# Kernel optimization log

Hardware: AMD Instinct MI355X
Metric: run time of the kernel (lower is better)

Reference implementation:

```python
import jax, jax.numpy as jnp
import numpy as np

N = 131072       # total nodes (B graphs x P nodes)
P = 4096         # nodes per graph
B = 32           # graphs in batch
E = 2097152      # edges (avg degree 16)
IN_DIM = 64
HID = 128
OUT = 16
EPS = 1e-5
SLOPE = 0.01


def _degrees(idx):
    # structural degree, clamped to min 1 (as DGL GraphConv does)
    d = jax.ops.segment_sum(jnp.ones((E,), jnp.float32), idx, num_segments=N)
    return jnp.maximum(d, 1.0)


def _graph_conv(x, W, src, dst, ew):
    # DGL GraphConv, norm='both', bias=False, with scalar edge weights:
    # h = D_out^{-1/2} x ; m_v = sum_{(u->v)} w_e h_u ; out = (D_in^{-1/2} m) W
    h = x * jax.lax.rsqrt(_degrees(src))[:, None]
    m = jax.ops.segment_sum(ew[:, None] * h[src], dst, num_segments=N)  # [N, F]
    return (m * jax.lax.rsqrt(_degrees(dst))[:, None]) @ W


def _graph_norm(x, gamma, beta, alpha):
    # GraphNorm (Cai et al. / PyG, batch=None): stats over all nodes per feature
    mu = jnp.mean(x, axis=0)
    c = x - alpha * mu
    var = jnp.mean(c * c, axis=0)
    return c * jax.lax.rsqrt(var + EPS) * gamma + beta


def _mean_nodes(h, gid):
    # per-graph mean readout; every graph has exactly P nodes
    return jax.ops.segment_sum(h, gid, num_segments=B) / P


def setup_inputs() -> dict:
    key = jax.random.key(0)
    ks = jax.random.split(key, 8)
    src = jax.random.randint(ks[0], (E,), 0, N, dtype=jnp.int32)
    # keep edges within each 4096-node graph block (batched DGL graph)
    dst = (src // P) * P + jax.random.randint(ks[1], (E,), 0, P, dtype=jnp.int32)
    features = jax.random.normal(ks[2], (N, IN_DIM), jnp.float32)
    edge_weights = jax.random.uniform(ks[3], (E,), jnp.float32)
    # kaiming/xavier-scale init approximations
    W1 = jax.random.normal(ks[4], (IN_DIM, HID), jnp.float32) * np.sqrt(2.0 / IN_DIM)
    W2 = jax.random.normal(ks[5], (HID, HID), jnp.float32) * np.sqrt(2.0 / HID)
    Wc = jax.random.normal(ks[6], (OUT, 2 * HID), jnp.float32) * np.sqrt(1.0 / (2 * HID))
    ones = jnp.ones((HID,), jnp.float32)
    zeros = jnp.zeros((HID,), jnp.float32)
    return {
        'features': features, 'edge_weights': edge_weights, 'src': src, 'dst': dst,
        'W1': W1, 'W2': W2, 'Wc': Wc,
        'gamma1': ones, 'beta1': zeros, 'alpha1': ones,
        'gamma2': ones, 'beta2': zeros, 'alpha2': ones,
    }


def reference(features, edge_weights, src, dst, W1, W2, Wc,
              gamma1, beta1, alpha1, gamma2, beta2, alpha2):
    gid = jnp.arange(N, dtype=jnp.int32) // P  # node -> graph id
    h1 = _graph_conv(features, W1, src, dst, edge_weights)
    h1 = jax.nn.leaky_relu(_graph_norm(h1, gamma1, beta1, alpha1), SLOPE)
    r1 = _mean_nodes(h1, gid)                  # [B, HID]
    h2 = _graph_conv(h1, W2, src, dst, edge_weights)
    h2 = jax.nn.leaky_relu(_graph_norm(h2, gamma2, beta2, alpha2), SLOPE)
    r2 = _mean_nodes(h2, gid)                  # [B, HID]
    readouts = jnp.concatenate([r1, r2], axis=1)  # [B, 2*HID]
    return readouts @ Wc.T                     # [B, OUT]
```

## Files before the change

### kernel.cpp

```cpp
#include <hip/hip_runtime.h>
#include <hip/hip_fp16.h>

constexpr int NN   = 131072;
constexpr int PP   = 4096;
constexpr int BG   = 32;
constexpr int EE   = 2097152;
constexpr int IND  = 64;
constexpr int HH   = 128;
constexpr int CAP  = 81920;
constexpr float EPSV   = 1e-5f;
constexpr float SLOPEV = 0.01f;

typedef short bf16x8 __attribute__((ext_vector_type(8)));
typedef float f32x4  __attribute__((ext_vector_type(4)));
typedef float f32x2  __attribute__((ext_vector_type(2)));

__device__ __forceinline__ unsigned f2bf(float f) {
    unsigned u = __float_as_uint(f);
    return (u + 0x7FFFu + ((u >> 16) & 1u)) >> 16;
}
__device__ __forceinline__ unsigned pack2bf(float lo, float hi) {
    return f2bf(lo) | (f2bf(hi) << 16);
}
__device__ __forceinline__ float bflo(unsigned p) { return __uint_as_float(p << 16); }
__device__ __forceinline__ float bfhi(unsigned p) { return __uint_as_float(p & 0xFFFF0000u); }
__device__ __forceinline__ float w16(unsigned r) {
    return __half2float(__ushort_as_half((unsigned short)(r >> 16)));
}

template <int K>
__device__ __forceinline__ void packw_body(const float* __restrict__ W,
                                           unsigned short* __restrict__ pw, int t) {
    if (t >= K * 16) return;
    int lane = t & 63, nt = (t >> 6) & 7, kt = t >> 9;
    int kbase = kt * 32 + ((lane >> 4) & 3) * 8;
    int col   = nt * 16 + (lane & 15);
    for (int j = 0; j < 8; j++)
        pw[t * 8 + j] = (unsigned short)f2bf(W[(kbase + j) * HH + col]);
}

__global__ __launch_bounds__(256) void k_prep(const float* __restrict__ features,
                                              unsigned* __restrict__ f8x,
                                              const float* __restrict__ W1,
                                              unsigned short* __restrict__ pw1,
                                              const float* __restrict__ W2,
                                              unsigned short* __restrict__ pw2,
                                              int* __restrict__ gcur,
                                              float* __restrict__ racc,
                                              unsigned* __restrict__ csr2) {
    int b = blockIdx.x, t = threadIdx.x;
    if (b < 8192) {
        int i = b * 256 + t;
        float4 v = ((const float4*)features)[i];
        int w0 = __builtin_amdgcn_cvt_pk_fp8_f32(v.x, v.y, 0, false);
        int w1 = __builtin_amdgcn_cvt_pk_fp8_f32(v.z, v.w, w0, true);
        f8x[i] = (unsigned)w1;
        return;
    }
    if (b == 8192) {
        if (t < BG) gcur[t * 16] = t * CAP;
        for (int i = t; i < 2 * BG * HH; i += 256) racc[i] = 0.f;
        return;
    }
    if (b < 8197) { packw_body<64>(W1, pw1, (b - 8193) * 256 + t); return; }
    if (b < 8205) { packw_body<128>(W2, pw2, (b - 8197) * 256 + t); return; }
    ((uint4*)csr2)[(b - 8205) * 256 + t] = make_uint4(0, 0, 0, 0);
}

__global__ __launch_bounds__(256) void k_part(const int* __restrict__ src,
                                              const int* __restrict__ dst,
                                              const float* __restrict__ ew,
                                              int* __restrict__ gcur,
                                              uint2* __restrict__ recs) {
    __shared__ int cnt[32];
    __shared__ int start[32];
    __shared__ int gbase[32];
    __shared__ uint2 stage[4096];
    int t = threadIdx.x;
    int ebase = blockIdx.x * 4096;
    if (t < 32) cnt[t] = 0;
    __syncthreads();
    int es[16]; int ed[16]; float ev[16];
#pragma unroll
    for (int k = 0; k < 16; k++) {
        int e = ebase + k * 256 + t;
        es[k] = src[e]; ed[k] = dst[e]; ev[k] = ew[e];
        atomicAdd(&cnt[es[k] >> 12], 1);
    }
    __syncthreads();
    if (t == 0) {
        int run = 0;
        for (int g = 0; g < 32; g++) { start[g] = run; run += cnt[g]; }
    }
    __syncthreads();
    if (t < 32) {
        gbase[t] = atomicAdd(&gcur[t * 16], cnt[t]);
        cnt[t] = start[t];
    }
    __syncthreads();
#pragma unroll
    for (int k = 0; k < 16; k++) {
        int g = es[k] >> 12;
        int pos = atomicAdd(&cnt[g], 1);
        stage[pos] = make_uint2((unsigned)(es[k] & 4095) | ((unsigned)(ed[k] & 4095) << 12) |
                                ((unsigned)g << 24), __float_as_uint(ev[k]));
    }
    __syncthreads();
    for (int i = t; i < 4096; i += 256) {
        uint2 r = stage[i];
        int g = r.x >> 24;
        recs[gbase[g] + (i - start[g])] = r;
    }
}

__global__ __launch_bounds__(1024) void k_hist(const uint2* __restrict__ recs,
                                               const int* __restrict__ gcur,
                                               int* __restrict__ shist,
                                               int* __restrict__ dhist) {
    __shared__ int hs[4096];
    __shared__ int hd[4096];
    int t = threadIdx.x;
    int g = blockIdx.x >> 3, c = blockIdx.x & 7;
    int n = gcur[g * 16] - g * CAP;
    int lo = (n * c) >> 3, hi = (n * (c + 1)) >> 3;
    ((int4*)hs)[t] = make_int4(0, 0, 0, 0);
    ((int4*)hd)[t] = make_int4(0, 0, 0, 0);
    __syncthreads();
    const uint2* base = recs + (size_t)g * CAP;
    for (int i = lo + t; i < hi; i += 1024) {
        unsigned x = base[i].x;
        atomicAdd(&hs[x & 4095], 1);
        atomicAdd(&hd[(x >> 12) & 4095], 1);
    }
    __syncthreads();
    ((int4*)(shist + (size_t)blockIdx.x * 4096))[t] = ((int4*)hs)[t];
    ((int4*)(dhist + (size_t)blockIdx.x * 4096))[t] = ((int4*)hd)[t];
}

__global__ __launch_bounds__(1024) void k_offs(int* __restrict__ shist,
                                               int* __restrict__ dhist,
                                               float* __restrict__ rs_s,
                                               float* __restrict__ rsd,
                                               int* __restrict__ degd,
                                               int* __restrict__ offs) {
    __shared__ int partial[1024];
    int t = threadIdx.x, g = blockIdx.x;
    int sdeg[4] = {0, 0, 0, 0}, ddeg[4] = {0, 0, 0, 0};
#pragma unroll
    for (int c = 0; c < 8; c++) {
        int4 sv = ((const int4*)(shist + (size_t)(g * 8 + c) * 4096))[t];
        int4 dv = ((const int4*)(dhist + (size_t)(g * 8 + c) * 4096))[t];
        sdeg[0] += sv.x; sdeg[1] += sv.y; sdeg[2] += sv.z; sdeg[3] += sv.w;
        ddeg[0] += dv.x; ddeg[1] += dv.y; ddeg[2] += dv.z; ddeg[3] += dv.w;
    }
    int pdeg[4];
#pragma unroll
    for (int j = 0; j < 4; j++) {
        int idx = t * 4 + j;
        int vs = sdeg[j]; if (vs < 1) vs = 1;
        rs_s[g * PP + idx] = rsqrtf((float)vs);
        int vd = ddeg[j]; if (vd < 1) vd = 1;
        rsd[g * PP + idx]  = rsqrtf((float)vd);
        pdeg[j] = (ddeg[j] + 3) & ~3;
        degd[g * PP + idx] = pdeg[j];
    }
    partial[t] = pdeg[0] + pdeg[1] + pdeg[2] + pdeg[3];
    __syncthreads();
    for (int off = 1; off < 1024; off <<= 1) {
        int v = partial[t];
        int add = (t >= off) ? partial[t - off] : 0;
        __syncthreads();
        partial[t] = v + add;
        __syncthreads();
    }
    int run = (t == 0) ? 0 : partial[t - 1];
#pragma unroll
    for (int j = 0; j < 4; j++) {
        int idx = t * 4 + j;
        offs[g * PP + idx] = g * CAP + run;
        int nb = run;
        for (int c = 0; c < 8; c++) {
            size_t hidx = (size_t)(g * 8 + c) * 4096 + idx;
            int v = dhist[hidx];
            dhist[hidx] = nb;
            nb += v;
        }
        run += pdeg[j];
    }
}

__global__ __launch_bounds__(1024) void k_place(const uint2* __restrict__ recs,
                                                const int* __restrict__ gcur,
                                                const int* __restrict__ dhist,
                                                const float* __restrict__ rs_s,
                                                unsigned* __restrict__ csr2) {
    __shared__ int cur[4096];
    __shared__ float rss[4096];
    int t = threadIdx.x;
    int g = blockIdx.x >> 3, c = blockIdx.x & 7;
    int n = gcur[g * 16] - g * CAP;
    int lo = (n * c) >> 3, hi = (n * (c + 1)) >> 3;
    ((int4*)cur)[t] = ((const int4*)(dhist + (size_t)blockIdx.x * 4096))[t];
    ((float4*)rss)[t] = ((const float4*)(rs_s + (size_t)g * PP))[t];
    __syncthreads();
    const uint2* base = recs + (size_t)g * CAP;
    unsigned* cbase = csr2 + (size_t)g * CAP;
    for (int i = lo + t; i < hi; i += 1024) {
        uint2 r = base[i];
        int sl = r.x & 4095, dl = (r.x >> 12) & 4095;
        int pos = atomicAdd(&cur[dl], 1);
        float wf = __uint_as_float(r.y) * rss[sl];
        cbase[pos] = (unsigned)sl | ((unsigned)__half_as_ushort(__float2half(wf)) << 16);
    }
}

__global__ __launch_bounds__(256) void k_aggemm1(const unsigned* __restrict__ f8x,
                                                 const unsigned* __restrict__ csr2,
                                                 const int* __restrict__ offs,
                                                 const int* __restrict__ degd,
                                                 const float* __restrict__ rsd,
                                                 const short* __restrict__ PW,
                                                 unsigned short* __restrict__ C,
                                                 float* __restrict__ part) {
    constexpr int WP = 36;
    __shared__ unsigned lds[64 * WP];
    __shared__ float s1[HH], s2[HH];
    int t = threadIdx.x;
    if (t < HH) { s1[t] = 0.f; s2[t] = 0.f; }
    int bid = blockIdx.x;
    int xcd = bid & 7, idx = bid >> 3;
    int g = xcd * 4 + (idx >> 6);
    int node0 = g * PP + (idx & 63) * 64;
    int lane = t & 63, wv = t >> 6;
    int q = lane >> 4, ql = lane & 15;
    const unsigned* hp8 = f8x + (size_t)((unsigned)(g * PP)) * 16 + ql;
    for (int p = 0; p < 2; p++) {
        int lrA = wv * 16 + p * 8 + q * 2;
        int va = node0 + lrA, vb = va + 1;
        int oa = offs[va], ca = degd[va];
        int ob = offs[vb], cb = degd[vb];
        float A0 = 0.f, A1 = 0.f, A2 = 0.f, A3 = 0.f;
        float B0 = 0.f, B1 = 0.f, B2 = 0.f, B3 = 0.f;
        int c0 = ca < cb ? ca : cb;
        int cm = ca < cb ? cb : ca;
        int i = 0;
        for (; i < c0; i += 4) {
            uint4 ra = *(const uint4*)(csr2 + oa + i);
            uint4 rb = *(const uint4*)(csr2 + ob + i);
            unsigned qa0 = hp8[(ra.x & 4095) * 16];
            unsigned qa1 = hp8[(ra.y & 4095) * 16];
            unsigned qa2 = hp8[(ra.z & 4095) * 16];
            unsigned qa3 = hp8[(ra.w & 4095) * 16];
            unsigned qb0 = hp8[(rb.x & 4095) * 16];
            unsigned qb1 = hp8[(rb.y & 4095) * 16];
            unsigned qb2 = hp8[(rb.z & 4095) * 16];
            unsigned qb3 = hp8[(rb.w & 4095) * 16];
            {
                f32x2 lo = __builtin_amdgcn_cvt_pk_f32_fp8((int)qa0, false);
                f32x2 hi = __builtin_amdgcn_cvt_pk_f32_fp8((int)qa0, true);
                float w = w16(ra.x);
                A0 += w * lo.x; A1 += w * lo.y; A2 += w * hi.x; A3 += w * hi.y;
            }
            {
                f32x2 lo = __builtin_amdgcn_cvt_pk_f32_fp8((int)qa1, false);
                f32x2 hi = __builtin_amdgcn_cvt_pk_f32_fp8((int)qa1, true);
                float w = w16(ra.y);
                A0 += w * lo.x; A1 += w * lo.y; A2 += w * hi.x; A3 += w * hi.y;
            }
            {
                f32x2 lo = __builtin_amdgcn_cvt_pk_f32_fp8((int)qa2, false);
                f32x2 hi = __builtin_amdgcn_cvt_pk_f32_fp8((int)qa2, true);
                float w = w16(ra.z);
                A0 += w * lo.x; A1 += w * lo.y; A2 += w * hi.x; A3 += w * hi.y;
            }
            {
                f32x2 lo = __builtin_amdgcn_cvt_pk_f32_fp8((int)qa3, false);
                f32x2 hi = __builtin_amdgcn_cvt_pk_f32_fp8((int)qa3, true);
                float w = w16(ra.w);
                A0 += w * lo.x; A1 += w * lo.y; A2 += w * hi.x; A3 += w * hi.y;
            }
            {
                f32x2 lo = __builtin_amdgcn_cvt_pk_f32_fp8((int)qb0, false);
                f32x2 hi = __builtin_amdgcn_cvt_pk_f32_fp8((int)qb0, true);
                float w = w16(rb.x);
                B0 += w * lo.x; B1 += w * lo.y; B2 += w * hi.x; B3 += w * hi.y;
            }
            {
                f32x2 lo = __builtin_amdgcn_cvt_pk_f32_fp8((int)qb1, false);
                f32x2 hi = __builtin_amdgcn_cvt_pk_f32_fp8((int)qb1, true);
                float w = w16(rb.y);
                B0 += w * lo.x; B1 += w * lo.y; B2 += w * hi.x; B3 += w * hi.y;
            }
            {
                f32x2 lo = __builtin_amdgcn_cvt_pk_f32_fp8((int)qb2, false);
                f32x2 hi = __builtin_amdgcn_cvt_pk_f32_fp8((int)qb2, true);
                float w = w16(rb.z);
                B0 += w * lo.x; B1 += w * lo.y; B2 += w * hi.x; B3 += w * hi.y;
            }
            {
                f32x2 lo = __builtin_amdgcn_cvt_pk_f32_fp8((int)qb3, false);
                f32x2 hi = __builtin_amdgcn_cvt_pk_f32_fp8((int)qb3, true);
                float w = w16(rb.w);
                B0 += w * lo.x; B1 += w * lo.y; B2 += w * hi.x; B3 += w * hi.y;
            }
        }
        if (i < cm) {
            int ot = (ca > cb) ? oa : ob;
            float E0 = 0.f, E1 = 0.f, E2 = 0.f, E3 = 0.f;
            for (; i < cm; i += 4) {
                uint4 rr = *(const uint4*)(csr2 + ot + i);
                unsigned q0 = hp8[(rr.x & 4095) * 16];
                unsigned q1 = hp8[(rr.y & 4095) * 16];
                unsigned q2 = hp8[(rr.z & 4095) * 16];
                unsigned q3 = hp8[(rr.w & 4095) * 16];
                {
                    f32x2 lo = __builtin_amdgcn_cvt_pk_f32_fp8((int)q0, false);
                    f32x2 hi = __builtin_amdgcn_cvt_pk_f32_fp8((int)q0, true);
                    float w = w16(rr.x);
                    E0 += w * lo.x; E1 += w * lo.y; E2 += w * hi.x; E3 += w * hi.y;
                }
                {
                    f32x2 lo = __builtin_amdgcn_cvt_pk_f32_fp8((int)q1, false);
                    f32x2 hi = __builtin_amdgcn_cvt_pk_f32_fp8((int)q1, true);
                    float w = w16(rr.y);
                    E0 += w * lo.x; E1 += w * lo.y; E2 += w * hi.x; E3 += w * hi.y;
                }
                {
                    f32x2 lo = __builtin_amdgcn_cvt_pk_f32_fp8((int)q2, false);
                    f32x2 hi = __builtin_amdgcn_cvt_pk_f32_fp8((int)q2, true);
                    float w = w16(rr.z);
                    E0 += w * lo.x; E1 += w * lo.y; E2 += w * hi.x; E3 += w * hi.y;
                }
                {
                    f32x2 lo = __builtin_amdgcn_cvt_pk_f32_fp8((int)q3, false);
                    f32x2 hi = __builtin_amdgcn_cvt_pk_f32_fp8((int)q3, true);
                    float w = w16(rr.w);
                    E0 += w * lo.x; E1 += w * lo.y; E2 += w * hi.x; E3 += w * hi.y;
                }
            }
            if (ca > cb) { A0 += E0; A1 += E1; A2 += E2; A3 += E3; }
            else         { B0 += E0; B1 += E1; B2 += E2; B3 += E3; }
        }
        float rda = rsd[va], rdb = rsd[vb];
        *(uint2*)&lds[lrA * WP + ql * 2] =
            make_uint2(pack2bf(A0 * rda, A1 * rda), pack2bf(A2 * rda, A3 * rda));
        *(uint2*)&lds[(lrA + 1) * WP + ql * 2] =
            make_uint2(pack2bf(B0 * rdb, B1 * rdb), pack2bf(B2 * rdb, B3 * rdb));
    }
    __syncthreads();
    int m = lane & 15, quad = lane >> 4;
    bf16x8 a[2];
#pragma unroll
    for (int kt = 0; kt < 2; kt++)
        a[kt] = *(const bf16x8*)&lds[(wv * 16 + m) * WP + kt * 16 + quad * 4];
#pragma unroll
    for (int nt = 0; nt < 8; nt++) {
        f32x4 acc = {0.f, 0.f, 0.f, 0.f};
#pragma unroll
        for (int kt = 0; kt < 2; kt++) {
            bf16x8 b = *(const bf16x8*)(PW + ((size_t)(kt * 8 + nt) * 64 + lane) * 8);
            acc = __builtin_amdgcn_mfma_f32_16x16x32_bf16(a[kt], b, acc, 0, 0, 0);
        }
        int col = nt * 16 + m;
        int r0 = node0 + wv * 16 + quad * 4;
        float ps = 0.f, pq = 0.f;
#pragma unroll
        for (int r = 0; r < 4; r++) {
            C[(size_t)(r0 + r) * HH + col] = (unsigned short)f2bf(acc[r]);
            ps += acc[r]; pq += acc[r] * acc[r];
        }
        atomicAdd(&s1[col], ps);
        atomicAdd(&s2[col], pq);
    }
    __syncthreads();
    if (t < HH) {
        part[bid * 256 + t]      = s1[t];
        part[bid * 256 + HH + t] = s2[t];
    }
}

__global__ __launch_bounds__(256) void k_aggemm2(const unsigned* __restrict__ f8,
                                                 const unsigned* __restrict__ csr2,
                                                 const int* __restrict__ offs,
                                                 const int* __restrict__ degd,
                                                 const float* __restrict__ rsd,
                                                 const short* __restrict__ PW,
                                                 unsigned short* __restrict__ C,
                                                 float* __restrict__ part) {
    constexpr int WP = 68;
    __shared__ unsigned lds[64 * WP];
    __shared__ float s1[HH], s2[HH];
    int t = threadIdx.x;
    if (t < HH) { s1[t] = 0.f; s2[t] = 0.f; }
    int bid = blockIdx.x;
    int xcd = bid & 7, idx = bid >> 3;
    int g = xcd * 4 + (idx >> 6);
    int node0 = g * PP + (idx & 63) * 64;
    int lane = t & 63, wv = t >> 6;
    int half = lane >> 5, sl = lane & 31;
    const unsigned* hp8 = f8 + (size_t)((unsigned)(g * PP)) * 32 + sl;
    for (int p = 0; p < 4; p++) {
        int va = node0 + wv * 16 + p * 4 + half * 2;
        int vb = va + 1;
        int oa = offs[va], ca = degd[va];
        int ob = offs[vb], cb = degd[vb];
        float A0 = 0.f, A1 = 0.f, A2 = 0.f, A3 = 0.f;
        float B0 = 0.f, B1 = 0.f, B2 = 0.f, B3 = 0.f;
        int c0 = ca < cb ? ca : cb;
        int cm = ca < cb ? cb : ca;
        int i = 0;
        for (; i < c0; i += 4) {
            uint4 ra = *(const uint4*)(csr2 + oa + i);
            uint4 rb = *(const uint4*)(csr2 + ob + i);
            unsigned qa0 = hp8[(ra.x & 4095) * 32];
            unsigned qa1 = hp8[(ra.y & 4095) * 32];
            unsigned qa2 = hp8[(ra.z & 4095) * 32];
            unsigned qa3 = hp8[(ra.w & 4095) * 32];
            unsigned qb0 = hp8[(rb.x & 4095) * 32];
            unsigned qb1 = hp8[(rb.y & 4095) * 32];
            unsigned qb2 = hp8[(rb.z & 4095) * 32];
            unsigned qb3 = hp8[(rb.w & 4095) * 32];
            {
                f32x2 lo = __builtin_amdgcn_cvt_pk_f32_fp8((int)qa0, false);
                f32x2 hi = __builtin_amdgcn_cvt_pk_f32_fp8((int)qa0, true);
                float w = w16(ra.x);
                A0 += w * lo.x; A1 += w * lo.y; A2 += w * hi.x; A3 += w * hi.y;
            }
            {
                f32x2 lo = __builtin_amdgcn_cvt_pk_f32_fp8((int)qa1, false);
                f32x2 hi = __builtin_amdgcn_cvt_pk_f32_fp8((int)qa1, true);
                float w = w16(ra.y);
                A0 += w * lo.x; A1 += w * lo.y; A2 += w * hi.x; A3 += w * hi.y;
            }
            {
                f32x2 lo = __builtin_amdgcn_cvt_pk_f32_fp8((int)qa2, false);
                f32x2 hi = __builtin_amdgcn_cvt_pk_f32_fp8((int)qa2, true);
                float w = w16(ra.z);
                A0 += w * lo.x; A1 += w * lo.y; A2 += w * hi.x; A3 += w * hi.y;
            }
            {
                f32x2 lo = __builtin_amdgcn_cvt_pk_f32_fp8((int)qa3, false);
                f32x2 hi = __builtin_amdgcn_cvt_pk_f32_fp8((int)qa3, true);
                float w = w16(ra.w);
                A0 += w * lo.x; A1 += w * lo.y; A2 += w * hi.x; A3 += w * hi.y;
            }
            {
                f32x2 lo = __builtin_amdgcn_cvt_pk_f32_fp8((int)qb0, false);
                f32x2 hi = __builtin_amdgcn_cvt_pk_f32_fp8((int)qb0, true);
                float w = w16(rb.x);
                B0 += w * lo.x; B1 += w * lo.y; B2 += w * hi.x; B3 += w * hi.y;
            }
            {
                f32x2 lo = __builtin_amdgcn_cvt_pk_f32_fp8((int)qb1, false);
                f32x2 hi = __builtin_amdgcn_cvt_pk_f32_fp8((int)qb1, true);
                float w = w16(rb.y);
                B0 += w * lo.x; B1 += w * lo.y; B2 += w * hi.x; B3 += w * hi.y;
            }
            {
                f32x2 lo = __builtin_amdgcn_cvt_pk_f32_fp8((int)qb2, false);
                f32x2 hi = __builtin_amdgcn_cvt_pk_f32_fp8((int)qb2, true);
                float w = w16(rb.z);
                B0 += w * lo.x; B1 += w * lo.y; B2 += w * hi.x; B3 += w * hi.y;
            }
            {
                f32x2 lo = __builtin_amdgcn_cvt_pk_f32_fp8((int)qb3, false);
                f32x2 hi = __builtin_amdgcn_cvt_pk_f32_fp8((int)qb3, true);
                float w = w16(rb.w);
                B0 += w * lo.x; B1 += w * lo.y; B2 += w * hi.x; B3 += w * hi.y;
            }
        }
        if (i < cm) {
            int ot = (ca > cb) ? oa : ob;
            float E0 = 0.f, E1 = 0.f, E2 = 0.f, E3 = 0.f;
            for (; i < cm; i += 4) {
                uint4 rr = *(const uint4*)(csr2 + ot + i);
                unsigned q0 = hp8[(rr.x & 4095) * 32];
                unsigned q1 = hp8[(rr.y & 4095) * 32];
                unsigned q2 = hp8[(rr.z & 4095) * 32];
                unsigned q3 = hp8[(rr.w & 4095) * 32];
                {
                    f32x2 lo = __builtin_amdgcn_cvt_pk_f32_fp8((int)q0, false);
                    f32x2 hi = __builtin_amdgcn_cvt_pk_f32_fp8((int)q0, true);
                    float w = w16(rr.x);
                    E0 += w * lo.x; E1 += w * lo.y; E2 += w * hi.x; E3 += w * hi.y;
                }
                {
                    f32x2 lo = __builtin_amdgcn_cvt_pk_f32_fp8((int)q1, false);
                    f32x2 hi = __builtin_amdgcn_cvt_pk_f32_fp8((int)q1, true);
                    float w = w16(rr.y);
                    E0 += w * lo.x; E1 += w * lo.y; E2 += w * hi.x; E3 += w * hi.y;
                }
                {
                    f32x2 lo = __builtin_amdgcn_cvt_pk_f32_fp8((int)q2, false);
                    f32x2 hi = __builtin_amdgcn_cvt_pk_f32_fp8((int)q2, true);
                    float w = w16(rr.z);
                    E0 += w * lo.x; E1 += w * lo.y; E2 += w * hi.x; E3 += w * hi.y;
                }
                {
                    f32x2 lo = __builtin_amdgcn_cvt_pk_f32_fp8((int)q3, false);
                    f32x2 hi = __builtin_amdgcn_cvt_pk_f32_fp8((int)q3, true);
                    float w = w16(rr.w);
                    E0 += w * lo.x; E1 += w * lo.y; E2 += w * hi.x; E3 += w * hi.y;
                }
            }
            if (ca > cb) { A0 += E0; A1 += E1; A2 += E2; A3 += E3; }
            else         { B0 += E0; B1 += E1; B2 += E2; B3 += E3; }
        }
        float rda = rsd[va], rdb = rsd[vb];
        int lrA = wv * 16 + p * 4 + half * 2;
        *(uint2*)&lds[lrA * WP + sl * 2] =
            make_uint2(pack2bf(A0 * rda, A1 * rda), pack2bf(A2 * rda, A3 * rda));
        *(uint2*)&lds[(lrA + 1) * WP + sl * 2] =
            make_uint2(pack2bf(B0 * rdb, B1 * rdb), pack2bf(B2 * rdb, B3 * rdb));
    }
    __syncthreads();
    int m = lane & 15, quad = lane >> 4;
    bf16x8 a[4];
#pragma unroll
    for (int kt = 0; kt < 4; kt++)
        a[kt] = *(const bf16x8*)&lds[(wv * 16 + m) * WP + kt * 16 + quad * 4];
#pragma unroll
    for (int nt = 0; nt < 8; nt++) {
        f32x4 acc = {0.f, 0.f, 0.f, 0.f};
#pragma unroll
        for (int kt = 0; kt < 4; kt++) {
            bf16x8 b = *(const bf16x8*)(PW + ((size_t)(kt * 8 + nt) * 64 + lane) * 8);
            acc = __builtin_amdgcn_mfma_f32_16x16x32_bf16(a[kt], b, acc, 0, 0, 0);
        }
        int col = nt * 16 + m;
        int r0 = node0 + wv * 16 + quad * 4;
        float ps = 0.f, pq = 0.f;
#pragma unroll
        for (int r = 0; r < 4; r++) {
            C[(size_t)(r0 + r) * HH + col] = (unsigned short)f2bf(acc[r]);
            ps += acc[r]; pq += acc[r] * acc[r];
        }
        atomicAdd(&s1[col], ps);
        atomicAdd(&s2[col], pq);
    }
    __syncthreads();
    if (t < HH) {
        part[bid * 256 + t]      = s1[t];
        part[bid * 256 + HH + t] = s2[t];
    }
}

__global__ __launch_bounds__(256) void k_red(const float* __restrict__ part,
                                             float* __restrict__ pb) {
    int t = threadIdx.x, b = blockIdx.x;
    float s = 0.f;
    for (int r = 0; r < 32; r++) s += part[(size_t)(b * 32 + r) * 256 + t];
    pb[b * 256 + t] = s;
}

__global__ void k_coef(const float* __restrict__ pb, const float* __restrict__ gamma,
                       const float* __restrict__ beta, const float* __restrict__ alpha,
                       float* __restrict__ ab) {
    int t = threadIdx.x;
    float s = 0.f;
    for (int b = 0; b < 64; b++) s += pb[b * 256 + t];
    __shared__ float sh[256];
    sh[t] = s;
    __syncthreads();
    if (t < 128) {
        float mu = sh[t] * (1.f / NN);
        float e2 = sh[128 + t] * (1.f / NN);
        float al = alpha[t];
        float var = e2 - (2.f * al - al * al) * mu * mu;
        float a = rsqrtf(var + EPSV) * gamma[t];
        ab[t] = a;
        ab[HH + t] = beta[t] - al * mu * a;
    }
}

template <bool WRITE>
__global__ __launch_bounds__(256) void k_normro(const unsigned* __restrict__ h,
                                                const float* __restrict__ ab,
                                                float* __restrict__ racc,
                                                unsigned short* __restrict__ f8) {
    int fp = threadIdx.x & 63;
    int q  = threadIdx.x >> 6;
    int node0 = blockIdx.x * 64;
    int g = node0 / PP;
    float a0 = ab[2 * fp], a1 = ab[2 * fp + 1];
    float b0 = ab[HH + 2 * fp], b1 = ab[HH + 2 * fp + 1];
    float s0 = 0.f, s1 = 0.f;
    for (int i = q; i < 64; i += 4) {
        size_t idx = (size_t)(node0 + i) * 64 + fp;
        unsigned v = h[idx];
        float x0 = fmaf(a0, bflo(v), b0); x0 = x0 > 0.f ? x0 : SLOPEV * x0;
        float x1 = fmaf(a1, bfhi(v), b1); x1 = x1 > 0.f ? x1 : SLOPEV * x1;
        if (WRITE) f8[idx] = (unsigned short)__builtin_amdgcn_cvt_pk_fp8_f32(x0, x1, 0, false);
        s0 += x0; s1 += x1;
    }
    __shared__ float sh[512];
    sh[threadIdx.x] = s0;
    sh[256 + threadIdx.x] = s1;
    __syncthreads();
    if (q == 0) {
        float t0 = s0 + sh[64 + fp] + sh[128 + fp] + sh[192 + fp];
        float t1 = s1 + sh[256 + 64 + fp] + sh[256 + 128 + fp] + sh[256 + 192 + fp];
        atomicAdd(&racc[g * HH + 2 * fp],     t0);
        atomicAdd(&racc[g * HH + 2 * fp + 1], t1);
    }
}

__global__ void k_final(const float* __restrict__ racc1, const float* __restrict__ racc2,
                        const float* __restrict__ Wc, float* __restrict__ out) {
    int t = threadIdx.x;
    int b = t >> 4, o = t & 15;
    float acc = 0.f;
    for (int f = 0; f < HH; f++) acc += racc1[b * HH + f] * Wc[o * (2 * HH) + f];
    for (int f = 0; f < HH; f++) acc += racc2[b * HH + f] * Wc[o * (2 * HH) + HH + f];
    out[t] = acc * (1.f / PP);
}

extern "C" void kernel_launch(void* const* d_in, const int* in_sizes, int n_in,
                              void* d_out, int out_size, void* d_ws, size_t ws_size,
                              hipStream_t stream) {
    const float* features = (const float*)d_in[0];
    const float* ew       = (const float*)d_in[1];
    const int*   src      = (const int*)d_in[2];
    const int*   dst      = (const int*)d_in[3];
    const float* W1       = (const float*)d_in[4];
    const float* W2       = (const float*)d_in[5];
    const float* Wc       = (const float*)d_in[6];
    const float* gamma1   = (const float*)d_in[7];
    const float* beta1    = (const float*)d_in[8];
    const float* alpha1   = (const float*)d_in[9];
    const float* gamma2   = (const float*)d_in[10];
    const float* beta2    = (const float*)d_in[11];
    const float* alpha2   = (const float*)d_in[12];
    float* out = (float*)d_out;

    char* w = (char*)d_ws;
    int*    gcur   = (int*)(w + 0);
    float*  racc1  = (float*)(w + (16u << 10));
    float*  racc2  = (float*)(w + (32u << 10));
    float*  ab1    = (float*)(w + (48u << 10));
    float*  ab2    = (float*)(w + (52u << 10));
    unsigned short* pw1 = (unsigned short*)(w + (64u << 10));
    unsigned short* pw2 = (unsigned short*)(w + (80u << 10));
    float*  pb     = (float*)(w + (128u << 10));
    float*  rs_s   = (float*)(w + (1024u << 10));
    float*  rsd    = (float*)(w + (1536u << 10));
    int*    degd   = (int*)(w + (2048u << 10));
    int*    offs   = (int*)(w + (2560u << 10));
    float*  part   = (float*)(w + (3u << 20));
    int*    shist  = (int*)(w + (5u << 20));
    int*    dhist  = (int*)(w + (9u << 20));
    unsigned* csr2 = (unsigned*)(w + (13u << 20));
    unsigned* mbuf = (unsigned*)(w + (23u << 20));
    unsigned* hbuf = (unsigned*)(w + (55u << 20));
    uint2*    recs = (uint2*)(w + (87u << 20));
    unsigned* f8x  = (unsigned*)(w + (107u << 20));
    unsigned* f8buf= (unsigned*)(w + (123u << 20));

    k_prep<<<10765, 256, 0, stream>>>(features, f8x, W1, pw1, W2, pw2, gcur, racc1, csr2);

    k_part<<<EE / 4096, 256, 0, stream>>>(src, dst, ew, gcur, recs);
    k_hist<<<BG * 8, 1024, 0, stream>>>(recs, gcur, shist, dhist);
    k_offs<<<BG, 1024, 0, stream>>>(shist, dhist, rs_s, rsd, degd, offs);
    k_place<<<BG * 8, 1024, 0, stream>>>(recs, gcur, dhist, rs_s, csr2);

    k_aggemm1<<<NN / 64, 256, 0, stream>>>(f8x, csr2, offs, degd, rsd,
                                           (const short*)pw1, (unsigned short*)hbuf, part);
    k_red<<<64, 256, 0, stream>>>(part, pb);
    k_coef<<<1, 256, 0, stream>>>(pb, gamma1, beta1, alpha1, ab1);
    k_normro<true><<<NN / 64, 256, 0, stream>>>(hbuf, ab1, racc1, (unsigned short*)f8buf);

    k_aggemm2<<<NN / 64, 256, 0, stream>>>(f8buf, csr2, offs, degd, rsd,
                                           (const short*)pw2, (unsigned short*)mbuf, part);
    k_red<<<64, 256, 0, stream>>>(part, pb);
    k_coef<<<1, 256, 0, stream>>>(pb, gamma2, beta2, alpha2, ab2);
    k_normro<false><<<NN / 64, 256, 0, stream>>>(mbuf, ab2, racc2, nullptr);

    k_final<<<1, 512, 0, stream>>>(racc1, racc2, Wc, out);
}
```

Measured before the change: 353.6 us.

## Fuse reduction/coef and readout/final kernels via tickets, unroll gather loops by eight

Merges k_red with k_coef and the second k_normro with k_final, using an atomic ticket so the last block finishes the dependent step. This removes three small kernel launches and the gaps between them. The edge-gather loops in both aggregation kernels get an 8-wide unrolled main loop, which puts more independent feature loads in flight per iteration. The normro kernels also switch to the XCD-aware block-to-graph mapping, which may change cache locality; the ticket counters add fences and atomics.

```diff
diff --git a/kernel.cpp b/kernel.cpp
--- a/kernel.cpp
+++ b/kernel.cpp
@@ -27,6 +27,13 @@
 __device__ __forceinline__ float w16(unsigned r) {
     return __half2float(__ushort_as_half((unsigned short)(r >> 16)));
 }
+__device__ __forceinline__ void edge_acc(float& a0, float& a1, float& a2, float& a3,
+                                         unsigned q, unsigned rec) {
+    f32x2 lo = __builtin_amdgcn_cvt_pk_f32_fp8((int)q, false);
+    f32x2 hi = __builtin_amdgcn_cvt_pk_f32_fp8((int)q, true);
+    float w = w16(rec);
+    a0 += w * lo.x; a1 += w * lo.y; a2 += w * hi.x; a3 += w * hi.y;
+}
 
 template <int K>
 __device__ __forceinline__ void packw_body(const float* __restrict__ W,
@@ -47,7 +54,8 @@
                                               unsigned short* __restrict__ pw2,
                                               int* __restrict__ gcur,
                                               float* __restrict__ racc,
-                                              unsigned* __restrict__ csr2) {
+                                              unsigned* __restrict__ csr2,
+                                              int* __restrict__ tickets) {
     int b = blockIdx.x, t = threadIdx.x;
     if (b < 8192) {
         int i = b * 256 + t;
@@ -59,6 +67,7 @@
     }
     if (b == 8192) {
         if (t < BG) gcur[t * 16] = t * CAP;
+        if (t < 48) tickets[t] = 0;
         for (int i = t; i < 2 * BG * HH; i += 256) racc[i] = 0.f;
         return;
     }
@@ -244,6 +253,44 @@
         int c0 = ca < cb ? ca : cb;
         int cm = ca < cb ? cb : ca;
         int i = 0;
+        for (; i + 8 <= c0; i += 8) {
+            uint4 ra0 = *(const uint4*)(csr2 + oa + i);
+            uint4 ra1 = *(const uint4*)(csr2 + oa + i + 4);
+            uint4 rb0 = *(const uint4*)(csr2 + ob + i);
+            uint4 rb1 = *(const uint4*)(csr2 + ob + i + 4);
+            unsigned qa0 = hp8[(ra0.x & 4095) * 16];
+            unsigned qa1 = hp8[(ra0.y & 4095) * 16];
+            unsigned qa2 = hp8[(ra0.z & 4095) * 16];
+            unsigned qa3 = hp8[(ra0.w & 4095) * 16];
+            unsigned qa4 = hp8[(ra1.x & 4095) * 16];
+            unsigned qa5 = hp8[(ra1.y & 4095) * 16];
+            unsigned qa6 = hp8[(ra1.z & 4095) * 16];
+            unsigned qa7 = hp8[(ra1.w & 4095) * 16];
+            unsigned qb0 = hp8[(rb0.x & 4095) * 16];
+            unsigned qb1 = hp8[(rb0.y & 4095) * 16];
+            unsigned qb2 = hp8[(rb0.z & 4095) * 16];
+            unsigned qb3 = hp8[(rb0.w & 4095) * 16];
+            unsigned qb4 = hp8[(rb1.x & 4095) * 16];
+            unsigned qb5 = hp8[(rb1.y & 4095) * 16];
+            unsigned qb6 = hp8[(rb1.z & 4095) * 16];
+            unsigned qb7 = hp8[(rb1.w & 4095) * 16];
+            edge_acc(A0, A1, A2, A3, qa0, ra0.x);
+            edge_acc(A0, A1, A2, A3, qa1, ra0.y);
+            edge_acc(A0, A1, A2, A3, qa2, ra0.z);
+            edge_acc(A0, A1, A2, A3, qa3, ra0.w);
+            edge_acc(A0, A1, A2, A3, qa4, ra1.x);
+            edge_acc(A0, A1, A2, A3, qa5, ra1.y);
+            edge_acc(A0, A1, A2, A3, qa6, ra1.z);
+            edge_acc(A0, A1, A2, A3, qa7, ra1.w);
+            edge_acc(B0, B1, B2, B3, qb0, rb0.x);
+            edge_acc(B0, B1, B2, B3, qb1, rb0.y);
+            edge_acc(B0, B1, B2, B3, qb2, rb0.z);
+            edge_acc(B0, B1, B2, B3, qb3, rb0.w);
+            edge_acc(B0, B1, B2, B3, qb4, rb1.x);
+            edge_acc(B0, B1, B2, B3, qb5, rb1.y);
+            edge_acc(B0, B1, B2, B3, qb6, rb1.z);
+            edge_acc(B0, B1, B2, B3, qb7, rb1.w);
+        }
         for (; i < c0; i += 4) {
             uint4 ra = *(const uint4*)(csr2 + oa + i);
             uint4 rb = *(const uint4*)(csr2 + ob + i);
@@ -255,54 +302,14 @@
             unsigned qb1 = hp8[(rb.y & 4095) * 16];
             unsigned qb2 = hp8[(rb.z & 4095) * 16];
             unsigned qb3 = hp8[(rb.w & 4095) * 16];
-            {
-                f32x2 lo = __builtin_amdgcn_cvt_pk_f32_fp8((int)qa0, false);
-                f32x2 hi = __builtin_amdgcn_cvt_pk_f32_fp8((int)qa0, true);
-                float w = w16(ra.x);
-                A0 += w * lo.x; A1 += w * lo.y; A2 += w * hi.x; A3 += w * hi.y;
-            }
-            {
-                f32x2 lo = __builtin_amdgcn_cvt_pk_f32_fp8((int)qa1, false);
-                f32x2 hi = __builtin_amdgcn_cvt_pk_f32_fp8((int)qa1, true);
-                float w = w16(ra.y);
-                A0 += w * lo.x; A1 += w * lo.y; A2 += w * hi.x; A3 += w * hi.y;
-            }
-            {
-                f32x2 lo = __builtin_amdgcn_cvt_pk_f32_fp8((int)qa2, false);
-                f32x2 hi = __builtin_amdgcn_cvt_pk_f32_fp8((int)qa2, true);
-                float w = w16(ra.z);
-                A0 += w * lo.x; A1 += w * lo.y; A2 += w * hi.x; A3 += w * hi.y;
-            }
-            {
-                f32x2 lo = __builtin_amdgcn_cvt_pk_f32_fp8((int)qa3, false);
-                f32x2 hi = __builtin_amdgcn_cvt_pk_f32_fp8((int)qa3, true);
-                float w = w16(ra.w);
-                A0 += w * lo.x; A1 += w * lo.y; A2 += w * hi.x; A3 += w * hi.y;
-            }
-            {
-                f32x2 lo = __builtin_amdgcn_cvt_pk_f32_fp8((int)qb0, false);
-                f32x2 hi = __builtin_amdgcn_cvt_pk_f32_fp8((int)qb0, true);
-                float w = w16(rb.x);
-                B0 += w * lo.x; B1 += w * lo.y; B2 += w * hi.x; B3 += w * hi.y;
-            }
-            {
-                f32x2 lo = __builtin_amdgcn_cvt_pk_f32_fp8((int)qb1, false);
-                f32x2 hi = __builtin_amdgcn_cvt_pk_f32_fp8((int)qb1, true);
-                float w = w16(rb.y);
-                B0 += w * lo.x; B1 += w * lo.y; B2 += w * hi.x; B3 += w * hi.y;
-            }
-            {
-                f32x2 lo = __builtin_amdgcn_cvt_pk_f32_fp8((int)qb2, false);
-                f32x2 hi = __builtin_amdgcn_cvt_pk_f32_fp8((int)qb2, true);
-                float w = w16(rb.z);
-                B0 += w * lo.x; B1 += w * lo.y; B2 += w * hi.x; B3 += w * hi.y;
-            }
-            {
-                f32x2 lo = __builtin_amdgcn_cvt_pk_f32_fp8((int)qb3, false);
-                f32x2 hi = __builtin_amdgcn_cvt_pk_f32_fp8((int)qb3, true);
-                float w = w16(rb.w);
-                B0 += w * lo.x; B1 += w * lo.y; B2 += w * hi.x; B3 += w * hi.y;
-            }
+            edge_acc(A0, A1, A2, A3, qa0, ra.x);
+            edge_acc(A0, A1, A2, A3, qa1, ra.y);
+            edge_acc(A0, A1, A2, A3, qa2, ra.z);
+            edge_acc(A0, A1, A2, A3, qa3, ra.w);
+            edge_acc(B0, B1, B2, B3, qb0, rb.x);
+            edge_acc(B0, B1, B2, B3, qb1, rb.y);
+            edge_acc(B0, B1, B2, B3, qb2, rb.z);
+            edge_acc(B0, B1, B2, B3, qb3, rb.w);
         }
         if (i < cm) {
             int ot = (ca > cb) ? oa : ob;
@@ -313,30 +320,10 @@
                 unsigned q1 = hp8[(rr.y & 4095) * 16];
                 unsigned q2 = hp8[(rr.z & 4095) * 16];
                 unsigned q3 = hp8[(rr.w & 4095) * 16];
-                {
-                    f32x2 lo = __builtin_amdgcn_cvt_pk_f32_fp8((int)q0, false);
-                    f32x2 hi = __builtin_amdgcn_cvt_pk_f32_fp8((int)q0, true);
-                    float w = w16(rr.x);
-                    E0 += w * lo.x; E1 += w * lo.y; E2 += w * hi.x; E3 += w * hi.y;
-                }
-                {
-                    f32x2 lo = __builtin_amdgcn_cvt_pk_f32_fp8((int)q1, false);
-                    f32x2 hi = __builtin_amdgcn_cvt_pk_f32_fp8((int)q1, true);
-                    float w = w16(rr.y);
-                    E0 += w * lo.x; E1 += w * lo.y; E2 += w * hi.x; E3 += w * hi.y;
-                }
-                {
-                    f32x2 lo = __builtin_amdgcn_cvt_pk_f32_fp8((int)q2, false);
-                    f32x2 hi = __builtin_amdgcn_cvt_pk_f32_fp8((int)q2, true);
-                    float w = w16(rr.z);
-                    E0 += w * lo.x; E1 += w * lo.y; E2 += w * hi.x; E3 += w * hi.y;
-                }
-                {
-                    f32x2 lo = __builtin_amdgcn_cvt_pk_f32_fp8((int)q3, false);
-                    f32x2 hi = __builtin_amdgcn_cvt_pk_f32_fp8((int)q3, true);
-                    float w = w16(rr.w);
-                    E0 += w * lo.x; E1 += w * lo.y; E2 += w * hi.x; E3 += w * hi.y;
-                }
+                edge_acc(E0, E1, E2, E3, q0, rr.x);
+                edge_acc(E0, E1, E2, E3, q1, rr.y);
+                edge_acc(E0, E1, E2, E3, q2, rr.z);
+                edge_acc(E0, E1, E2, E3, q3, rr.w);
             }
             if (ca > cb) { A0 += E0; A1 += E1; A2 += E2; A3 += E3; }
             else         { B0 += E0; B1 += E1; B2 += E2; B3 += E3; }
@@ -400,8 +387,8 @@
     int half = lane >> 5, sl = lane & 31;
     const unsigned* hp8 = f8 + (size_t)((unsigned)(g * PP)) * 32 + sl;
     for (int p = 0; p < 4; p++) {
-        int va = node0 + wv * 16 + p * 4 + half * 2;
-        int vb = va + 1;
+        int lrA = wv * 16 + p * 4 + half * 2;
+        int va = node0 + lrA, vb = va + 1;
         int oa = offs[va], ca = degd[va];
         int ob = offs[vb], cb = degd[vb];
         float A0 = 0.f, A1 = 0.f, A2 = 0.f, A3 = 0.f;
@@ -409,6 +396,44 @@
         int c0 = ca < cb ? ca : cb;
         int cm = ca < cb ? cb : ca;
         int i = 0;
+        for (; i + 8 <= c0; i += 8) {
+            uint4 ra0 = *(const uint4*)(csr2 + oa + i);
+            uint4 ra1 = *(const uint4*)(csr2 + oa + i + 4);
+            uint4 rb0 = *(const uint4*)(csr2 + ob + i);
+            uint4 rb1 = *(const uint4*)(csr2 + ob + i + 4);
+            unsigned qa0 = hp8[(ra0.x & 4095) * 32];
+            unsigned qa1 = hp8[(ra0.y & 4095) * 32];
+            unsigned qa2 = hp8[(ra0.z & 4095) * 32];
+            unsigned qa3 = hp8[(ra0.w & 4095) * 32];
+            unsigned qa4 = hp8[(ra1.x & 4095) * 32];
+            unsigned qa5 = hp8[(ra1.y & 4095) * 32];
+            unsigned qa6 = hp8[(ra1.z & 4095) * 32];
+            unsigned qa7 = hp8[(ra1.w & 4095) * 32];
+            unsigned qb0 = hp8[(rb0.x & 4095) * 32];
+            unsigned qb1 = hp8[(rb0.y & 4095) * 32];
+            unsigned qb2 = hp8[(rb0.z & 4095) * 32];
+            unsigned qb3 = hp8[(rb0.w & 4095) * 32];
+            unsigned qb4 = hp8[(rb1.x & 4095) * 32];
+            unsigned qb5 = hp8[(rb1.y & 4095) * 32];
+            unsigned qb6 = hp8[(rb1.z & 4095) * 32];
+            unsigned qb7 = hp8[(rb1.w & 4095) * 32];
+            edge_acc(A0, A1, A2, A3, qa0, ra0.x);
+            edge_acc(A0, A1, A2, A3, qa1, ra0.y);
+            edge_acc(A0, A1, A2, A3, qa2, ra0.z);
+            edge_acc(A0, A1, A2, A3, qa3, ra0.w);
+            edge_acc(A0, A1, A2, A3, qa4, ra1.x);
+            edge_acc(A0, A1, A2, A3, qa5, ra1.y);
+            edge_acc(A0, A1, A2, A3, qa6, ra1.z);
+            edge_acc(A0, A1, A2, A3, qa7, ra1.w);
+            edge_acc(B0, B1, B2, B3, qb0, rb0.x);
+            edge_acc(B0, B1, B2, B3, qb1, rb0.y);
+            edge_acc(B0, B1, B2, B3, qb2, rb0.z);
+            edge_acc(B0, B1, B2, B3, qb3, rb0.w);
+            edge_acc(B0, B1, B2, B3, qb4, rb1.x);
+            edge_acc(B0, B1, B2, B3, qb5, rb1.y);
+            edge_acc(B0, B1, B2, B3, qb6, rb1.z);
+            edge_acc(B0, B1, B2, B3, qb7, rb1.w);
+        }
         for (; i < c0; i += 4) {
             uint4 ra = *(const uint4*)(csr2 + oa + i);
             uint4 rb = *(const uint4*)(csr2 + ob + i);
@@ -420,54 +445,14 @@
             unsigned qb1 = hp8[(rb.y & 4095) * 32];
             unsigned qb2 = hp8[(rb.z & 4095) * 32];
             unsigned qb3 = hp8[(rb.w & 4095) * 32];
-            {
-                f32x2 lo = __builtin_amdgcn_cvt_pk_f32_fp8((int)qa0, false);
-                f32x2 hi = __builtin_amdgcn_cvt_pk_f32_fp8((int)qa0, true);
-                float w = w16(ra.x);
-                A0 += w * lo.x; A1 += w * lo.y; A2 += w * hi.x; A3 += w * hi.y;
-            }
-            {
-                f32x2 lo = __builtin_amdgcn_cvt_pk_f32_fp8((int)qa1, false);
-                f32x2 hi = __builtin_amdgcn_cvt_pk_f32_fp8((int)qa1, true);
-                float w = w16(ra.y);
-                A0 += w * lo.x; A1 += w * lo.y; A2 += w * hi.x; A3 += w * hi.y;
-            }
-            {
-                f32x2 lo = __builtin_amdgcn_cvt_pk_f32_fp8((int)qa2, false);
-                f32x2 hi = __builtin_amdgcn_cvt_pk_f32_fp8((int)qa2, true);
-                float w = w16(ra.z);
-                A0 += w * lo.x; A1 += w * lo.y; A2 += w * hi.x; A3 += w * hi.y;
-            }
-            {
-                f32x2 lo = __builtin_amdgcn_cvt_pk_f32_fp8((int)qa3, false);
-                f32x2 hi = __builtin_amdgcn_cvt_pk_f32_fp8((int)qa3, true);
-                float w = w16(ra.w);
-                A0 += w * lo.x; A1 += w * lo.y; A2 += w * hi.x; A3 += w * hi.y;
-            }
-            {
-                f32x2 lo = __builtin_amdgcn_cvt_pk_f32_fp8((int)qb0, false);
-                f32x2 hi = __builtin_amdgcn_cvt_pk_f32_fp8((int)qb0, true);
-                float w = w16(rb.x);
-                B0 += w * lo.x; B1 += w * lo.y; B2 += w * hi.x; B3 += w * hi.y;
-            }
-            {
-                f32x2 lo = __builtin_amdgcn_cvt_pk_f32_fp8((int)qb1, false);
-                f32x2 hi = __builtin_amdgcn_cvt_pk_f32_fp8((int)qb1, true);
-                float w = w16(rb.y);
-                B0 += w * lo.x; B1 += w * lo.y; B2 += w * hi.x; B3 += w * hi.y;
-            }
-            {
-                f32x2 lo = __builtin_amdgcn_cvt_pk_f32_fp8((int)qb2, false);
-                f32x2 hi = __builtin_amdgcn_cvt_pk_f32_fp8((int)qb2, true);
-                float w = w16(rb.z);
-                B0 += w * lo.x; B1 += w * lo.y; B2 += w * hi.x; B3 += w * hi.y;
-            }
-            {
-                f32x2 lo = __builtin_amdgcn_cvt_pk_f32_fp8((int)qb3, false);
-                f32x2 hi = __builtin_amdgcn_cvt_pk_f32_fp8((int)qb3, true);
-                float w = w16(rb.w);
-                B0 += w * lo.x; B1 += w * lo.y; B2 += w * hi.x; B3 += w * hi.y;
-            }
+            edge_acc(A0, A1, A2, A3, qa0, ra.x);
+            edge_acc(A0, A1, A2, A3, qa1, ra.y);
+            edge_acc(A0, A1, A2, A3, qa2, ra.z);
+            edge_acc(A0, A1, A2, A3, qa3, ra.w);
+            edge_acc(B0, B1, B2, B3, qb0, rb.x);
+            edge_acc(B0, B1, B2, B3, qb1, rb.y);
+            edge_acc(B0, B1, B2, B3, qb2, rb.z);
+            edge_acc(B0, B1, B2, B3, qb3, rb.w);
         }
         if (i < cm) {
             int ot = (ca > cb) ? oa : ob;
@@ -478,36 +463,15 @@
                 unsigned q1 = hp8[(rr.y & 4095) * 32];
                 unsigned q2 = hp8[(rr.z & 4095) * 32];
                 unsigned q3 = hp8[(rr.w & 4095) * 32];
-                {
-                    f32x2 lo = __builtin_amdgcn_cvt_pk_f32_fp8((int)q0, false);
-                    f32x2 hi = __builtin_amdgcn_cvt_pk_f32_fp8((int)q0, true);
-                    float w = w16(rr.x);
-                    E0 += w * lo.x; E1 += w * lo.y; E2 += w * hi.x; E3 += w * hi.y;
-                }
-                {
-                    f32x2 lo = __builtin_amdgcn_cvt_pk_f32_fp8((int)q1, false);
-                    f32x2 hi = __builtin_amdgcn_cvt_pk_f32_fp8((int)q1, true);
-                    float w = w16(rr.y);
-                    E0 += w * lo.x; E1 += w * lo.y; E2 += w * hi.x; E3 += w * hi.y;
-                }
-                {
-                    f32x2 lo = __builtin_amdgcn_cvt_pk_f32_fp8((int)q2, false);
-                    f32x2 hi = __builtin_amdgcn_cvt_pk_f32_fp8((int)q2, true);
-                    float w = w16(rr.z);
-                    E0 += w * lo.x; E1 += w * lo.y; E2 += w * hi.x; E3 += w * hi.y;
-                }
-                {
-                    f32x2 lo = __builtin_amdgcn_cvt_pk_f32_fp8((int)q3, false);
-                    f32x2 hi = __builtin_amdgcn_cvt_pk_f32_fp8((int)q3, true);
-                    float w = w16(rr.w);
-                    E0 += w * lo.x; E1 += w * lo.y; E2 += w * hi.x; E3 += w * hi.y;
-                }
+                edge_acc(E0, E1, E2, E3, q0, rr.x);
+                edge_acc(E0, E1, E2, E3, q1, rr.y);
+                edge_acc(E0, E1, E2, E3, q2, rr.z);
+                edge_acc(E0, E1, E2, E3, q3, rr.w);
             }
             if (ca > cb) { A0 += E0; A1 += E1; A2 += E2; A3 += E3; }
             else         { B0 += E0; B1 += E1; B2 += E2; B3 += E3; }
         }
         float rda = rsd[va], rdb = rsd[vb];
-        int lrA = wv * 16 + p * 4 + half * 2;
         *(uint2*)&lds[lrA * WP + sl * 2] =
             make_uint2(pack2bf(A0 * rda, A1 * rda), pack2bf(A2 * rda, A3 * rda));
         *(uint2*)&lds[(lrA + 1) * WP + sl * 2] =
@@ -545,22 +509,28 @@
     }
 }
 
-__global__ __launch_bounds__(256) void k_red(const float* __restrict__ part,
-                                             float* __restrict__ pb) {
+__global__ __launch_bounds__(256) void k_redcoef(const float* __restrict__ part,
+                                                 float* __restrict__ pb,
+                                                 const float* __restrict__ gamma,
+                                                 const float* __restrict__ beta,
+                                                 const float* __restrict__ alpha,
+                                                 float* __restrict__ ab,
+                                                 int* __restrict__ ticket) {
     int t = threadIdx.x, b = blockIdx.x;
     float s = 0.f;
     for (int r = 0; r < 32; r++) s += part[(size_t)(b * 32 + r) * 256 + t];
     pb[b * 256 + t] = s;
-}
-
-__global__ void k_coef(const float* __restrict__ pb, const float* __restrict__ gamma,
-                       const float* __restrict__ beta, const float* __restrict__ alpha,
-                       float* __restrict__ ab) {
-    int t = threadIdx.x;
-    float s = 0.f;
-    for (int b = 0; b < 64; b++) s += pb[b * 256 + t];
+    __threadfence();
+    __syncthreads();
+    __shared__ int last;
+    if (t == 0) last = (atomicAdd(ticket, 1) == 63);
+    __syncthreads();
+    if (!last) return;
+    __threadfence();
+    float s2 = 0.f;
+    for (int b2 = 0; b2 < 64; b2++) s2 += pb[b2 * 256 + t];
     __shared__ float sh[256];
-    sh[t] = s;
+    sh[t] = s2;
     __syncthreads();
     if (t < 128) {
         float mu = sh[t] * (1.f / NN);
@@ -573,24 +543,25 @@
     }
 }
 
-template <bool WRITE>
-__global__ __launch_bounds__(256) void k_normro(const unsigned* __restrict__ h,
-                                                const float* __restrict__ ab,
-                                                float* __restrict__ racc,
-                                                unsigned short* __restrict__ f8) {
+__global__ __launch_bounds__(256) void k_normro1(const unsigned* __restrict__ h,
+                                                 const float* __restrict__ ab,
+                                                 float* __restrict__ racc,
+                                                 unsigned short* __restrict__ f8) {
     int fp = threadIdx.x & 63;
     int q  = threadIdx.x >> 6;
-    int node0 = blockIdx.x * 64;
-    int g = node0 / PP;
+    int bid = blockIdx.x;
+    int xcd = bid & 7, idx = bid >> 3;
+    int g = xcd * 4 + (idx >> 6);
+    int node0 = g * PP + (idx & 63) * 64;
     float a0 = ab[2 * fp], a1 = ab[2 * fp + 1];
     float b0 = ab[HH + 2 * fp], b1 = ab[HH + 2 * fp + 1];
     float s0 = 0.f, s1 = 0.f;
     for (int i = q; i < 64; i += 4) {
-        size_t idx = (size_t)(node0 + i) * 64 + fp;
-        unsigned v = h[idx];
+        size_t idx2 = (size_t)(node0 + i) * 64 + fp;
+        unsigned v = h[idx2];
         float x0 = fmaf(a0, bflo(v), b0); x0 = x0 > 0.f ? x0 : SLOPEV * x0;
         float x1 = fmaf(a1, bfhi(v), b1); x1 = x1 > 0.f ? x1 : SLOPEV * x1;
-        if (WRITE) f8[idx] = (unsigned short)__builtin_amdgcn_cvt_pk_fp8_f32(x0, x1, 0, false);
+        f8[idx2] = (unsigned short)__builtin_amdgcn_cvt_pk_fp8_f32(x0, x1, 0, false);
         s0 += x0; s1 += x1;
     }
     __shared__ float sh[512];
@@ -605,14 +576,54 @@
     }
 }
 
-__global__ void k_final(const float* __restrict__ racc1, const float* __restrict__ racc2,
-                        const float* __restrict__ Wc, float* __restrict__ out) {
+__global__ __launch_bounds__(256) void k_normro_final(const unsigned* __restrict__ h,
+                                                      const float* __restrict__ ab,
+                                                      float* __restrict__ racc2,
+                                                      const float* __restrict__ racc1,
+                                                      const float* __restrict__ Wc,
+                                                      float* __restrict__ out,
+                                                      int* __restrict__ ticket) {
+    int fp = threadIdx.x & 63;
+    int q  = threadIdx.x >> 6;
+    int bid = blockIdx.x;
+    int xcd = bid & 7, idx = bid >> 3;
+    int g = xcd * 4 + (idx >> 6);
+    int node0 = g * PP + (idx & 63) * 64;
+    float a0 = ab[2 * fp], a1 = ab[2 * fp + 1];
+    float b0 = ab[HH + 2 * fp], b1 = ab[HH + 2 * fp + 1];
+    float s0 = 0.f, s1 = 0.f;
+    for (int i = q; i < 64; i += 4) {
+        size_t idx2 = (size_t)(node0 + i) * 64 + fp;
+        unsigned v = h[idx2];
+        float x0 = fmaf(a0, bflo(v), b0); x0 = x0 > 0.f ? x0 : SLOPEV * x0;
+        float x1 = fmaf(a1, bfhi(v), b1); x1 = x1 > 0.f ? x1 : SLOPEV * x1;
+        s0 += x0; s1 += x1;
+    }
+    __shared__ float sh[512];
+    sh[threadIdx.x] = s0;
+    sh[256 + threadIdx.x] = s1;
+    __syncthreads();
+    if (q == 0) {
+        float t0 = s0 + sh[64 + fp] + sh[128 + fp] + sh[192 + fp];
+        float t1 = s1 + sh[256 + 64 + fp] + sh[256 + 128 + fp] + sh[256 + 192 + fp];
+        atomicAdd(&racc2[g * HH + 2 * fp],     t0);
+        atomicAdd(&racc2[g * HH + 2 * fp + 1], t1);
+    }
+    __threadfence();
+    __syncthreads();
+    __shared__ int last;
+    if (threadIdx.x == 0) last = (atomicAdd(ticket, 1) == 2047);
+    __syncthreads();
+    if (!last) return;
+    __threadfence();
     int t = threadIdx.x;
-    int b = t >> 4, o = t & 15;
-    float acc = 0.f;
-    for (int f = 0; f < HH; f++) acc += racc1[b * HH + f] * Wc[o * (2 * HH) + f];
-    for (int f = 0; f < HH; f++) acc += racc2[b * HH + f] * Wc[o * (2 * HH) + HH + f];
-    out[t] = acc * (1.f / PP);
+    for (int u = t; u < 512; u += 256) {
+        int b = u >> 4, o = u & 15;
+        float acc = 0.f;
+        for (int f = 0; f < HH; f++) acc += racc1[b * HH + f] * Wc[o * (2 * HH) + f];
+        for (int f = 0; f < HH; f++) acc += racc2[b * HH + f] * Wc[o * (2 * HH) + HH + f];
+        out[u] = acc * (1.f / PP);
+    }
 }
 
 extern "C" void kernel_launch(void* const* d_in, const int* in_sizes, int n_in,
@@ -639,6 +650,7 @@
     float*  racc2  = (float*)(w + (32u << 10));
     float*  ab1    = (float*)(w + (48u << 10));
     float*  ab2    = (float*)(w + (52u << 10));
+    int*    tk     = (int*)(w + (56u << 10));
     unsigned short* pw1 = (unsigned short*)(w + (64u << 10));
     unsigned short* pw2 = (unsigned short*)(w + (80u << 10));
     float*  pb     = (float*)(w + (128u << 10));
@@ -656,7 +668,7 @@
     unsigned* f8x  = (unsigned*)(w + (107u << 20));
     unsigned* f8buf= (unsigned*)(w + (123u << 20));
 
-    k_prep<<<10765, 256, 0, stream>>>(features, f8x, W1, pw1, W2, pw2, gcur, racc1, csr2);
+    k_prep<<<10765, 256, 0, stream>>>(features, f8x, W1, pw1, W2, pw2, gcur, racc1, csr2, tk);
 
     k_part<<<EE / 4096, 256, 0, stream>>>(src, dst, ew, gcur, recs);
     k_hist<<<BG * 8, 1024, 0, stream>>>(recs, gcur, shist, dhist);
@@ -665,15 +677,11 @@
 
     k_aggemm1<<<NN / 64, 256, 0, stream>>>(f8x, csr2, offs, degd, rsd,
                                            (const short*)pw1, (unsigned short*)hbuf, part);
-    k_red<<<64, 256, 0, stream>>>(part, pb);
-    k_coef<<<1, 256, 0, stream>>>(pb, gamma1, beta1, alpha1, ab1);
-    k_normro<true><<<NN / 64, 256, 0, stream>>>(hbuf, ab1, racc1, (unsigned short*)f8buf);
+    k_redcoef<<<64, 256, 0, stream>>>(part, pb, gamma1, beta1, alpha1, ab1, tk + 0);
+    k_normro1<<<NN / 64, 256, 0, stream>>>(hbuf, ab1, racc1, (unsigned short*)f8buf);
 
     k_aggemm2<<<NN / 64, 256, 0, stream>>>(f8buf, csr2, offs, degd, rsd,
                                            (const short*)pw2, (unsigned short*)mbuf, part);
-    k_red<<<64, 256, 0, stream>>>(part, pb);
-    k_coef<<<1, 256, 0, stream>>>(pb, gamma2, beta2, alpha2, ab2);
-    k_normro<false><<<NN / 64, 256, 0, stream>>>(mbuf, ab2, racc2, nullptr);
-
-    k_final<<<1, 512, 0, stream>>>(racc1, racc2, Wc, out);
-}
+    k_redcoef<<<64, 256, 0, stream>>>(part, pb, gamma2, beta2, alpha2, ab2, tk + 16);
+    k_normro_final<<<NN / 64, 256, 0, stream>>>(mbuf, ab2, racc2, racc1, Wc, out, tk + 32);
+}
```

Measured after the change: 484.5 us. 1.37x slower.
